# Performance work log

Hardware: AMD Instinct MI355X
Metric: run time of the kernel (lower is better)

## Reference

```python
import jax, jax.numpy as jnp
import numpy as np

EPS = 1e-5
NEG = -1e22

def layernorm(x, g, b):
    m = jnp.mean(x, axis=-1, keepdims=True)
    v = jnp.mean((x - m) ** 2, axis=-1, keepdims=True)
    return (x - m) * jax.lax.rsqrt(v + EPS) * g + b

def setup_inputs() -> dict:
    key = jax.random.key(0)
    ks = jax.random.split(key, 16)
    B, N, D, K = 4, 2048, 512, 32
    H = int(D * 1.5)  # 768
    sc = lambda fan_in: 1.0 / np.sqrt(fan_in)
    inp = {
        'x': jax.random.normal(ks[0], (B, N, D), jnp.float32),
        'adj': jax.random.uniform(ks[1], (B, N, N), jnp.float32),
        'inxs': jax.random.randint(ks[2], (B, N, K), 0, N, jnp.int64),
        'Wq': jax.random.normal(ks[3], (D, D), jnp.float32) * sc(D),
        'bq': jnp.zeros((D,), jnp.float32),
        'Wk': jax.random.normal(ks[4], (D, D), jnp.float32) * sc(D),
        'bk': jnp.zeros((D,), jnp.float32),
        'Wv': jax.random.normal(ks[5], (D, D), jnp.float32) * sc(D),
        'bv': jnp.zeros((D,), jnp.float32),
        'Wo': jax.random.normal(ks[6], (D, D), jnp.float32) * sc(D),
        'bo': jnp.zeros((D,), jnp.float32),
        'g1': jnp.ones((D,), jnp.float32),
        'beta1': jnp.zeros((D,), jnp.float32),
        'W1': jax.random.normal(ks[7], (D, H), jnp.float32) * sc(D),
        'bf1': jnp.zeros((H,), jnp.float32),
        'W2': jax.random.normal(ks[8], (H, D), jnp.float32) * sc(H),
        'bf2': jnp.zeros((D,), jnp.float32),
        'g2': jnp.ones((D,), jnp.float32),
        'beta2': jnp.zeros((D,), jnp.float32),
    }
    return inp

def reference(x, adj, inxs, Wq, bq, Wk, bk, Wv, bv, Wo, bo, g1, beta1, W1, bf1, W2, bf2, g2, beta2):
    B, N, D = x.shape
    # projections
    q = x @ Wq + bq                                   # [B,N,D]
    k = x @ Wk + bk
    v = x @ Wv + bv
    # gather top-k neighbor keys/values: [B,N,K,D]
    b_idx = jnp.arange(B)[:, None, None]
    k_nei = k[b_idx, inxs]
    v_nei = v[b_idx, inxs]
    # attention over selected neighbors, masked by adjacency sign
    scores = jnp.einsum('bnd,bnkd->bnk', q, k_nei) / jnp.sqrt(jnp.float32(D))
    adj_nei = jnp.take_along_axis(adj, inxs, axis=2)  # [B,N,K]
    mask = jnp.where(adj_nei > 0, 0.0, NEG)
    attn = jax.nn.softmax(scores + mask, axis=-1)
    att_out = jnp.einsum('bnk,bnkd->bnd', attn, v_nei) @ Wo + bo
    # residual + LN
    y = layernorm(x + jax.nn.relu(att_out), g1, beta1)
    # FFN + residual + LN
    h = jax.nn.relu(y @ W1 + bf1) @ W2 + bf2
    return layernorm(y + h, g2, beta2)
```

## Files before the change

kernel.cpp:

```cpp
#include <hip/hip_runtime.h>
#include <stdint.h>

typedef __attribute__((ext_vector_type(8))) short short8;
typedef __attribute__((ext_vector_type(4))) float f32x4;
typedef __attribute__((ext_vector_type(2))) _Float16 h2;
typedef __attribute__((ext_vector_type(8))) _Float16 half8;

#define QSCALE 21.1666667f
#define SCONST 9.86413e-5f

static __device__ __forceinline__ unsigned short f2bf(float f) {
  unsigned int u = __float_as_uint(f);
  u += 0x7FFFu + ((u >> 16) & 1u);
  return (unsigned short)(u >> 16);
}
static __device__ __forceinline__ float bf2f(unsigned short h) {
  return __uint_as_float(((unsigned int)h) << 16);
}
static __device__ __forceinline__ unsigned short f2h(float f) {
  _Float16 h = (_Float16)f;
  return __builtin_bit_cast(unsigned short, h);
}
static __device__ __forceinline__ float hdot2(unsigned int a, unsigned int b, float c) {
  return __builtin_amdgcn_fdot2(__builtin_bit_cast(h2, a), __builtin_bit_cast(h2, b), c, false);
}
static __device__ __forceinline__ signed char q8(float v) {
  float sv = fminf(fmaxf(v * QSCALE, -127.f), 127.f);
  return (signed char)(int)rintf(sv);
}

#define GLD16(gp, lp) __builtin_amdgcn_global_load_lds( \
    (__attribute__((address_space(1))) void*)(gp), \
    (__attribute__((address_space(3))) void*)(lp), 16, 0, 0)

__global__ __launch_bounds__(256) void k_prep(
    const float* __restrict__ adj, const int* __restrict__ inxs,
    float* __restrict__ maskb, const float* __restrict__ x,
    unsigned short* __restrict__ xb,
    const float* __restrict__ Wq, const float* __restrict__ Wk,
    const float* __restrict__ Wv, const float* __restrict__ Wo,
    const float* __restrict__ W1, const float* __restrict__ W2,
    unsigned short* __restrict__ wqkvt, unsigned short* __restrict__ wot,
    unsigned short* __restrict__ w1t, unsigned short* __restrict__ w2t) {
  __shared__ float tile[32][33];
  const int bid = blockIdx.x;
  const int t = threadIdx.x;
  if (bid < 1024) {
    const int xcd = bid & 7;
    const int bb = xcd >> 1;
    const int s = ((bid >> 3) << 1) | (xcd & 1);
    const long row = ((long)bb << 11) | ((long)s << 3) | (t >> 5);
    const int kk = t & 31;
    const int idx = inxs[row * 32 + kk];
    const float a = adj[row * 2048 + idx];
    maskb[row * 32 + kk] = a > 0.f ? 0.f : -1e22f;
    return;
  }
  if (bid < 3072) {
    const int lb = bid - 1024;
    const int xcd = lb & 7;
    const int bb = xcd >> 1;
    const int s = ((lb >> 3) << 1) | (xcd & 1);
    const long row = ((long)bb << 11) | ((long)s << 2) | (t >> 6);
    const int lane = t & 63;
    const float4* p = (const float4*)(x + row * 512 + lane * 8);
    float4 a = p[0], b = p[1];
    short8 v;
    v[0] = (short)f2h(a.x); v[1] = (short)f2h(a.y);
    v[2] = (short)f2h(a.z); v[3] = (short)f2h(a.w);
    v[4] = (short)f2h(b.x); v[5] = (short)f2h(b.y);
    v[6] = (short)f2h(b.z); v[7] = (short)f2h(b.w);
    *(short8*)(xb + row * 512 + lane * 8) = v;
    return;
  }
  const int lb = bid - 3072;
  const float* src;
  unsigned short* dst;
  int R, C, f16, local;
  if (lb < 768) {
    const int m = lb >> 8;
    src = m == 0 ? Wq : (m == 1 ? Wk : Wv);
    dst = wqkvt + (long)m * 512 * 512;
    R = 512; C = 512; f16 = 1; local = lb & 255;
  } else if (lb < 1024) {
    src = Wo; dst = wot; R = 512; C = 512; f16 = 0; local = lb - 768;
  } else if (lb < 1408) {
    src = W1; dst = w1t; R = 512; C = 768; f16 = 0; local = lb - 1024;
  } else {
    src = W2; dst = w2t; R = 768; C = 512; f16 = 0; local = lb - 1408;
  }
  const int ntx = C >> 5;
  const int c0 = (local % ntx) << 5;
  const int r0 = (local / ntx) << 5;
  const int tx = t & 31, ty = t >> 5;
#pragma unroll
  for (int i = 0; i < 4; i++)
    tile[ty + i * 8][tx] = src[(long)(r0 + ty + i * 8) * C + c0 + tx];
  __syncthreads();
#pragma unroll
  for (int i = 0; i < 4; i++) {
    float v = tile[tx][ty + i * 8];
    dst[(long)(c0 + ty + i * 8) * R + r0 + tx] = f16 ? f2h(v) : f2bf(v);
  }
}

__global__ __launch_bounds__(256) void k_gemm_qkv(
    const unsigned short* __restrict__ A, const unsigned short* __restrict__ Bt,
    const float* __restrict__ bq, const float* __restrict__ bk,
    const float* __restrict__ bv, signed char* __restrict__ qk8,
    unsigned short* __restrict__ vh) {
  const int K = 512;
  __shared__ unsigned short As[2][128 * 64];
  __shared__ unsigned short Bs[2][128 * 64];
  const int t = threadIdx.x;
  const int lane = t & 63;
  const int w = t >> 6;
  const int wr = w >> 1, wc = w & 1;
  const int lin = blockIdx.x;
  const int xcd = lin & 7;
  const int bb = xcd >> 1;
  const int s = ((lin >> 3) << 1) | (xcd & 1);
  const int m0 = (bb * 16 + s / 12) * 128;
  const int n0 = (s % 12) * 128;

  f32x4 acc[4][4];
#pragma unroll
  for (int mi = 0; mi < 4; mi++)
#pragma unroll
    for (int ni = 0; ni < 4; ni++) {
      f32x4 z = {0.f, 0.f, 0.f, 0.f};
      acc[mi][ni] = z;
    }

  auto stage = [&](int buf, int k0) {
#pragma unroll
    for (int i = 0; i < 4; i++) {
      const int c = t + i * 256;
      const int r = c >> 3, j = c & 7;
      GLD16(A + (long)(m0 + r) * K + k0 + ((j ^ (r & 7)) << 3), &As[buf][c * 8]);
    }
#pragma unroll
    for (int i = 0; i < 4; i++) {
      const int c = t + i * 256;
      const int r = c >> 3, j = c & 7;
      GLD16(Bt + (long)(n0 + r) * K + k0 + ((j ^ (r & 7)) << 3), &Bs[buf][c * 8]);
    }
  };

  const int nt = K >> 6;
  stage(0, 0);
  for (int tt = 0; tt < nt; ++tt) {
    const int cur = tt & 1;
    if (tt + 1 < nt) {
      stage(cur ^ 1, (tt + 1) << 6);
      asm volatile("s_waitcnt vmcnt(8)" ::: "memory");
    } else {
      asm volatile("s_waitcnt vmcnt(0)" ::: "memory");
    }
    __builtin_amdgcn_s_barrier();

#pragma unroll
    for (int kk = 0; kk < 2; kk++) {
      short8 af[4], bf[4];
#pragma unroll
      for (int mi = 0; mi < 4; mi++) {
        const int r = wr * 64 + mi * 16 + (lane & 15);
        const int jj = (kk << 2) + (lane >> 4);
        af[mi] = *(const short8*)&As[cur][r * 64 + ((jj ^ (r & 7)) << 3)];
      }
#pragma unroll
      for (int ni = 0; ni < 4; ni++) {
        const int r = wc * 64 + ni * 16 + (lane & 15);
        const int jj = (kk << 2) + (lane >> 4);
        bf[ni] = *(const short8*)&Bs[cur][r * 64 + ((jj ^ (r & 7)) << 3)];
      }
#pragma unroll
      for (int mi = 0; mi < 4; mi++)
#pragma unroll
        for (int ni = 0; ni < 4; ni++)
          acc[mi][ni] = __builtin_amdgcn_mfma_f32_16x16x32_f16(
              __builtin_bit_cast(half8, af[mi]), __builtin_bit_cast(half8, bf[ni]),
              acc[mi][ni], 0, 0, 0);
    }
    asm volatile("s_waitcnt lgkmcnt(0)" ::: "memory");
    __builtin_amdgcn_s_barrier();
  }

  const int lr = (lane >> 4) * 4;
  const int lc = lane & 15;
  if (n0 < 1024) {
#pragma unroll
    for (int mi = 0; mi < 4; mi++) {
#pragma unroll
      for (int ni = 0; ni < 4; ni++) {
        const int col = n0 + wc * 64 + ni * 16 + lc;
        const float bvv = col < 512 ? bq[col] : bk[col - 512];
#pragma unroll
        for (int r = 0; r < 4; r++) {
          const int row = m0 + wr * 64 + mi * 16 + lr + r;
          qk8[(long)row * 1024 + col] = q8(acc[mi][ni][r] + bvv);
        }
      }
    }
  } else {
#pragma unroll
    for (int mi = 0; mi < 4; mi++) {
#pragma unroll
      for (int ni = 0; ni < 4; ni++) {
        const int col = n0 + wc * 64 + ni * 16 + lc;
        const float bvv = bv[col - 1024];
#pragma unroll
        for (int r = 0; r < 4; r++) {
          const int row = m0 + wr * 64 + mi * 16 + lr + r;
          vh[(long)row * 512 + (col - 1024)] = f2h(acc[mi][ni][r] + bvv);
        }
      }
    }
  }
}

template <int EPI>
__global__ __launch_bounds__(256) void k_gemm(const unsigned short* __restrict__ A,
                                              const unsigned short* __restrict__ Bt,
                                              const float* __restrict__ bias,
                                              unsigned short* __restrict__ C,
                                              int M, int N, int K) {
  __shared__ unsigned short As[2][128 * 64];
  __shared__ unsigned short Bs[2][64 * 64];
  const int t = threadIdx.x;
  const int lane = t & 63;
  const int w = t >> 6;
  const int wr = w >> 1, wc = w & 1;
  const int lin = blockIdx.x;
  const int xcd = lin & 7;
  const int bb = xcd >> 1;
  const int nx = N >> 6;
  const int s = ((lin >> 3) << 1) | (xcd & 1);
  const int m0 = (bb * 16 + s / nx) * 128;
  const int n0 = (s % nx) * 64;

  f32x4 acc[4][2];
#pragma unroll
  for (int mi = 0; mi < 4; mi++)
#pragma unroll
    for (int ni = 0; ni < 2; ni++) {
      f32x4 z = {0.f, 0.f, 0.f, 0.f};
      acc[mi][ni] = z;
    }

  auto stage = [&](int buf, int k0) {
#pragma unroll
    for (int i = 0; i < 4; i++) {
      const int c = t + i * 256;
      const int r = c >> 3, j = c & 7;
      GLD16(A + (long)(m0 + r) * K + k0 + ((j ^ (r & 7)) << 3), &As[buf][c * 8]);
    }
#pragma unroll
    for (int i = 0; i < 2; i++) {
      const int c = t + i * 256;
      const int r = c >> 3, j = c & 7;
      GLD16(Bt + (long)(n0 + r) * K + k0 + ((j ^ (r & 7)) << 3), &Bs[buf][c * 8]);
    }
  };

  const int nt = K >> 6;
  stage(0, 0);
  for (int tt = 0; tt < nt; ++tt) {
    const int cur = tt & 1;
    if (tt + 1 < nt) {
      stage(cur ^ 1, (tt + 1) << 6);
      asm volatile("s_waitcnt vmcnt(6)" ::: "memory");
    } else {
      asm volatile("s_waitcnt vmcnt(0)" ::: "memory");
    }
    __builtin_amdgcn_s_barrier();

#pragma unroll
    for (int kk = 0; kk < 2; kk++) {
      short8 af[4], bf[2];
#pragma unroll
      for (int mi = 0; mi < 4; mi++) {
        const int r = wr * 64 + mi * 16 + (lane & 15);
        const int jj = (kk << 2) + (lane >> 4);
        af[mi] = *(const short8*)&As[cur][r * 64 + ((jj ^ (r & 7)) << 3)];
      }
#pragma unroll
      for (int ni = 0; ni < 2; ni++) {
        const int r = wc * 32 + ni * 16 + (lane & 15);
        const int jj = (kk << 2) + (lane >> 4);
        bf[ni] = *(const short8*)&Bs[cur][r * 64 + ((jj ^ (r & 7)) << 3)];
      }
#pragma unroll
      for (int mi = 0; mi < 4; mi++)
#pragma unroll
        for (int ni = 0; ni < 2; ni++)
          acc[mi][ni] = __builtin_amdgcn_mfma_f32_16x16x32_bf16(af[mi], bf[ni], acc[mi][ni], 0, 0, 0);
    }
    asm volatile("s_waitcnt lgkmcnt(0)" ::: "memory");
    __builtin_amdgcn_s_barrier();
  }

  const int lr = (lane >> 4) * 4;
  const int lc = lane & 15;
#pragma unroll
  for (int mi = 0; mi < 4; mi++) {
#pragma unroll
    for (int ni = 0; ni < 2; ni++) {
      const int col = n0 + wc * 32 + ni * 16 + lc;
      const float bvv = bias[col];
#pragma unroll
      for (int r = 0; r < 4; r++) {
        const int row = m0 + wr * 64 + mi * 16 + lr + r;
        float v = acc[mi][ni][r] + bvv;
        if (EPI == 1) v = fmaxf(v, 0.f);
        C[(long)row * N + col] = f2bf(v);
      }
    }
  }
}

__global__ __launch_bounds__(256, 8) void k_attn(const signed char* __restrict__ qk8,
                                                 const unsigned short* __restrict__ vh,
                                                 const float* __restrict__ maskb,
                                                 const int* __restrict__ inxs,
                                                 unsigned short* __restrict__ att) {
  const int t = threadIdx.x;
  const int lane = t & 63;
  const int w = t >> 6;
  const int bid = blockIdx.x;
  const int xcd = bid & 7;
  const int b = xcd >> 1;
  const int sub = ((bid >> 3) << 1) | (xcd & 1);
  const int row = (b << 11) | (sub << 2) | w;
  const long base = (long)b * 2048;
  const int g = lane >> 4;
  const int li = lane & 15;
  const int kk = lane & 31;

  const int* ix = inxs + (long)row * 32;
  const int ixv = ix[kk];
  const float mval = maskb[(long)row * 32 + kk];

  const uint2* qp = (const uint2*)(qk8 + (long)row * 1024);
  uint2 qc[4];
#pragma unroll
  for (int c = 0; c < 4; c++) qc[c] = qp[li + c * 16];

  float scr[8];
#pragma unroll
  for (int r = 0; r < 8; r++) {
    const int nb = __shfl(ixv, r * 4 + g, 64);
    const uint2* kp = (const uint2*)(qk8 + (base + nb) * 1024 + 512);
    int di = 0;
#pragma unroll
    for (int c = 0; c < 4; c++) {
      uint2 kc = kp[li + c * 16];
      di = __builtin_amdgcn_sdot4((int)kc.x, (int)qc[c].x, di, false);
      di = __builtin_amdgcn_sdot4((int)kc.y, (int)qc[c].y, di, false);
    }
#pragma unroll
    for (int m = 1; m <= 8; m <<= 1) di += __shfl_xor(di, m, 64);
    scr[r] = (float)di;
  }

  const int srcl = (kk & 3) << 4;
  float s = __shfl(scr[0], srcl, 64);
#pragma unroll
  for (int r = 1; r < 8; r++) {
    const float tr = __shfl(scr[r], srcl, 64);
    s = ((kk >> 2) == r) ? tr : s;
  }
  s = s * SCONST + mval;

  float mx = s;
#pragma unroll
  for (int d = 1; d <= 16; d <<= 1) mx = fmaxf(mx, __shfl_xor(mx, d, 64));
  const float e = __expf(s - mx);
  float ts = e;
#pragma unroll
  for (int d = 1; d <= 16; d <<= 1) ts += __shfl_xor(ts, d, 64);
  const float inv = 1.f / ts;

  float o[8] = {0, 0, 0, 0, 0, 0, 0, 0};
#pragma unroll
  for (int p = 0; p < 16; p++) {
    const int u0 = __shfl(ixv, 2 * p, 64);
    const int u1 = __shfl(ixv, 2 * p + 1, 64);
    const uint4 v0c = *(const uint4*)(vh + (base + u0) * 512 + lane * 8);
    const uint4 v1c = *(const uint4*)(vh + (base + u1) * 512 + lane * 8);
    const float pe0 = __shfl(e, 2 * p, 64);
    const float pe1 = __shfl(e, 2 * p + 1, 64);
    const unsigned int pp =
        __builtin_bit_cast(unsigned int, __builtin_amdgcn_cvt_pkrtz(pe0, pe1));
    const unsigned int vw0[4] = {v0c.x, v0c.y, v0c.z, v0c.w};
    const unsigned int vw1[4] = {v1c.x, v1c.y, v1c.z, v1c.w};
#pragma unroll
    for (int q = 0; q < 4; q++) {
      const unsigned int even = __builtin_amdgcn_perm(vw1[q], vw0[q], 0x05040100u);
      const unsigned int odd  = __builtin_amdgcn_perm(vw1[q], vw0[q], 0x07060302u);
      o[2 * q]     = hdot2(even, pp, o[2 * q]);
      o[2 * q + 1] = hdot2(odd,  pp, o[2 * q + 1]);
    }
  }

  short8 ov;
#pragma unroll
  for (int j = 0; j < 8; j++) ov[j] = (short)f2bf(o[j] * inv);
  *(short8*)(att + (long)row * 512 + lane * 8) = ov;
}

__global__ __launch_bounds__(256) void k_ln1(const float* __restrict__ x,
                                             const unsigned short* __restrict__ o,
                                             const float* __restrict__ g,
                                             const float* __restrict__ beta,
                                             unsigned short* __restrict__ y) {
  const int lane = threadIdx.x & 63;
  const int w = threadIdx.x >> 6;
  const int bid = blockIdx.x;
  const int xcd = bid & 7;
  const int bb = xcd >> 1;
  const int s0 = ((bid >> 3) << 1) | (xcd & 1);
  const long row = ((long)bb << 11) | ((long)s0 << 2) | w;
  const float4* xp = (const float4*)(x + row * 512 + lane * 8);
  float4 x0 = xp[0], x1 = xp[1];
  short8 ov = *(const short8*)(o + row * 512 + lane * 8);
  float tv[8] = {x0.x, x0.y, x0.z, x0.w, x1.x, x1.y, x1.z, x1.w};
  float s = 0.f, s2 = 0.f;
#pragma unroll
  for (int j = 0; j < 8; j++) {
    tv[j] += bf2f((unsigned short)ov[j]);
    s += tv[j];
    s2 += tv[j] * tv[j];
  }
#pragma unroll
  for (int m = 32; m >= 1; m >>= 1) {
    s += __shfl_xor(s, m, 64);
    s2 += __shfl_xor(s2, m, 64);
  }
  const float mean = s * (1.f / 512.f);
  const float var = s2 * (1.f / 512.f) - mean * mean;
  const float r = rsqrtf(var + 1e-5f);
  const float4* gp = (const float4*)(g + lane * 8);
  const float4* bp = (const float4*)(beta + lane * 8);
  float4 g0 = gp[0], g1v = gp[1], b0 = bp[0], b1 = bp[1];
  float gg[8] = {g0.x, g0.y, g0.z, g0.w, g1v.x, g1v.y, g1v.z, g1v.w};
  float bb2[8] = {b0.x, b0.y, b0.z, b0.w, b1.x, b1.y, b1.z, b1.w};
  short8 yv;
#pragma unroll
  for (int j = 0; j < 8; j++) yv[j] = (short)f2bf((tv[j] - mean) * r * gg[j] + bb2[j]);
  *(short8*)(y + row * 512 + lane * 8) = yv;
}

__global__ __launch_bounds__(256) void k_ln2(const unsigned short* __restrict__ y,
                                             const unsigned short* __restrict__ f,
                                             const float* __restrict__ g,
                                             const float* __restrict__ beta,
                                             float* __restrict__ out) {
  const int lane = threadIdx.x & 63;
  const int w = threadIdx.x >> 6;
  const int bid = blockIdx.x;
  const int xcd = bid & 7;
  const int bb = xcd >> 1;
  const int s0 = ((bid >> 3) << 1) | (xcd & 1);
  const long row = ((long)bb << 11) | ((long)s0 << 2) | w;
  short8 yv = *(const short8*)(y + row * 512 + lane * 8);
  short8 fv = *(const short8*)(f + row * 512 + lane * 8);
  float tv[8];
  float s = 0.f, s2 = 0.f;
#pragma unroll
  for (int j = 0; j < 8; j++) {
    tv[j] = bf2f((unsigned short)yv[j]) + bf2f((unsigned short)fv[j]);
    s += tv[j];
    s2 += tv[j] * tv[j];
  }
#pragma unroll
  for (int m = 32; m >= 1; m >>= 1) {
    s += __shfl_xor(s, m, 64);
    s2 += __shfl_xor(s2, m, 64);
  }
  const float mean = s * (1.f / 512.f);
  const float var = s2 * (1.f / 512.f) - mean * mean;
  const float r = rsqrtf(var + 1e-5f);
  const float4* gp = (const float4*)(g + lane * 8);
  const float4* bp = (const float4*)(beta + lane * 8);
  float4 g0 = gp[0], g1v = gp[1], b0 = bp[0], b1 = bp[1];
  float gg[8] = {g0.x, g0.y, g0.z, g0.w, g1v.x, g1v.y, g1v.z, g1v.w};
  float bb2[8] = {b0.x, b0.y, b0.z, b0.w, b1.x, b1.y, b1.z, b1.w};
  float ovv[8];
#pragma unroll
  for (int j = 0; j < 8; j++) ovv[j] = (tv[j] - mean) * r * gg[j] + bb2[j];
  float4* op = (float4*)(out + row * 512 + lane * 8);
  float4 o0 = {ovv[0], ovv[1], ovv[2], ovv[3]};
  float4 o1 = {ovv[4], ovv[5], ovv[6], ovv[7]};
  op[0] = o0;
  op[1] = o1;
}

extern "C" void kernel_launch(void* const* d_in, const int* in_sizes, int n_in,
                              void* d_out, int out_size, void* d_ws, size_t ws_size,
                              hipStream_t stream) {
  const float* x   = (const float*)d_in[0];
  const float* adj = (const float*)d_in[1];
  const int*   inx = (const int*)d_in[2];
  const float* Wq  = (const float*)d_in[3];
  const float* bq  = (const float*)d_in[4];
  const float* Wk  = (const float*)d_in[5];
  const float* bk  = (const float*)d_in[6];
  const float* Wv  = (const float*)d_in[7];
  const float* bv  = (const float*)d_in[8];
  const float* Wo  = (const float*)d_in[9];
  const float* bo  = (const float*)d_in[10];
  const float* g1  = (const float*)d_in[11];
  const float* be1 = (const float*)d_in[12];
  const float* W1  = (const float*)d_in[13];
  const float* bf1 = (const float*)d_in[14];
  const float* W2  = (const float*)d_in[15];
  const float* bf2 = (const float*)d_in[16];
  const float* g2  = (const float*)d_in[17];
  const float* be2 = (const float*)d_in[18];

  unsigned short* xb    = (unsigned short*)d_ws;
  unsigned short* wqkvt = xb + 4194304;
  unsigned short* wot   = wqkvt + 786432;
  unsigned short* w1t   = wot + 262144;
  unsigned short* w2t   = w1t + 393216;
  signed char*    qk8   = (signed char*)(w2t + 393216);
  unsigned short* vh    = (unsigned short*)(qk8 + 8388608);
  unsigned short* oproj = vh + 4194304;
  unsigned short* y     = oproj + 4194304;
  float*          maskb = (float*)(y + 4194304);
  unsigned short* att   = xb;
  unsigned short* h     = (unsigned short*)qk8;
  unsigned short* f     = oproj;

  k_prep<<<4864, 256, 0, stream>>>(adj, inx, maskb, x, xb, Wq, Wk, Wv, Wo, W1, W2,
                                   wqkvt, wot, w1t, w2t);

  k_gemm_qkv<<<768, 256, 0, stream>>>(xb, wqkvt, bq, bk, bv, qk8, vh);
  k_attn<<<2048, 256, 0, stream>>>(qk8, vh, maskb, inx, att);
  k_gemm<1><<<512, 256, 0, stream>>>(att, wot, bo, oproj, 8192, 512, 512);
  k_ln1<<<2048, 256, 0, stream>>>(x, oproj, g1, be1, y);
  k_gemm<1><<<768, 256, 0, stream>>>(y, w1t, bf1, h, 8192, 768, 512);
  k_gemm<0><<<512, 256, 0, stream>>>(h, w2t, bf2, f, 8192, 512, 768);
  k_ln2<<<2048, 256, 0, stream>>>(y, f, g2, be2, (float*)d_out);
}
```

Before: 105.8 us.

## Quantize V to per-row uint8 for attention and widen GEMM N-tile to 128

Adds a kernel that quantizes the fp16 V rows to unsigned 8-bit with a per-row scale and offset. The attention kernel then gathers 8 bytes per lane instead of 16 and corrects the offset with a weighted-sum term, which halves the gather traffic of the neighbour V reads. Separately, the generic GEMM tile grows from 128x64 to 128x128, giving each wave more MFMA work per LDS load and halving the grid sizes. The costs are an extra launch and pass over V, reduced precision in the attention output, and higher register and LDS use in the GEMM, which may lower occupancy.

```diff
diff --git a/kernel.cpp b/kernel.cpp
--- a/kernel.cpp
+++ b/kernel.cpp
@@ -21,12 +21,15 @@
   _Float16 h = (_Float16)f;
   return __builtin_bit_cast(unsigned short, h);
 }
-static __device__ __forceinline__ float hdot2(unsigned int a, unsigned int b, float c) {
-  return __builtin_amdgcn_fdot2(__builtin_bit_cast(h2, a), __builtin_bit_cast(h2, b), c, false);
+static __device__ __forceinline__ float h2f(unsigned short h) {
+  return (float)__builtin_bit_cast(_Float16, h);
 }
 static __device__ __forceinline__ signed char q8(float v) {
   float sv = fminf(fmaxf(v * QSCALE, -127.f), 127.f);
   return (signed char)(int)rintf(sv);
+}
+static __device__ __forceinline__ float ub(unsigned int x, int n) {
+  return (float)((x >> (8 * n)) & 0xffu);
 }
 
 #define GLD16(gp, lp) __builtin_amdgcn_global_load_lds( \
@@ -219,6 +222,43 @@
   }
 }
 
+__global__ __launch_bounds__(256) void k_qv(const unsigned short* __restrict__ vh,
+                                            unsigned char* __restrict__ v8,
+                                            float* __restrict__ vs) {
+  const int bid = blockIdx.x;
+  const int xcd = bid & 7;
+  const int bb = xcd >> 1;
+  const int s0 = ((bid >> 3) << 1) | (xcd & 1);
+  const long row = ((long)bb << 11) | ((long)s0 << 2) | (threadIdx.x >> 6);
+  const int lane = threadIdx.x & 63;
+  const unsigned short* vp = vh + row * 512 + lane * 8;
+  float vf[8];
+#pragma unroll
+  for (int j = 0; j < 8; j++) vf[j] = h2f(vp[j]);
+  float mx = 0.f;
+#pragma unroll
+  for (int j = 0; j < 8; j++) mx = fmaxf(mx, fabsf(vf[j]));
+#pragma unroll
+  for (int d = 1; d <= 32; d <<= 1) mx = fmaxf(mx, __shfl_xor(mx, d, 64));
+  mx = fmaxf(mx, 1e-8f);
+  const float sc = mx * (1.f / 127.f);
+  const float isc = 127.f / mx;
+  unsigned int w0 = 0, w1 = 0;
+#pragma unroll
+  for (int j = 0; j < 4; j++) {
+    unsigned int u = (unsigned int)(int)rintf(fminf(fmaxf(vf[j] * isc + 128.f, 0.f), 255.f));
+    w0 |= (u & 255u) << (8 * j);
+  }
+#pragma unroll
+  for (int j = 0; j < 4; j++) {
+    unsigned int u = (unsigned int)(int)rintf(fminf(fmaxf(vf[4 + j] * isc + 128.f, 0.f), 255.f));
+    w1 |= (u & 255u) << (8 * j);
+  }
+  uint2 pw = {w0, w1};
+  *(uint2*)(v8 + row * 512 + lane * 8) = pw;
+  if (lane == 0) vs[row] = sc;
+}
+
 template <int EPI>
 __global__ __launch_bounds__(256) void k_gemm(const unsigned short* __restrict__ A,
                                               const unsigned short* __restrict__ Bt,
@@ -226,7 +266,7 @@
                                               unsigned short* __restrict__ C,
                                               int M, int N, int K) {
   __shared__ unsigned short As[2][128 * 64];
-  __shared__ unsigned short Bs[2][64 * 64];
+  __shared__ unsigned short Bs[2][128 * 64];
   const int t = threadIdx.x;
   const int lane = t & 63;
   const int w = t >> 6;
@@ -234,16 +274,16 @@
   const int lin = blockIdx.x;
   const int xcd = lin & 7;
   const int bb = xcd >> 1;
-  const int nx = N >> 6;
+  const int nx = N >> 7;
   const int s = ((lin >> 3) << 1) | (xcd & 1);
   const int m0 = (bb * 16 + s / nx) * 128;
-  const int n0 = (s % nx) * 64;
-
-  f32x4 acc[4][2];
+  const int n0 = (s % nx) * 128;
+
+  f32x4 acc[4][4];
 #pragma unroll
   for (int mi = 0; mi < 4; mi++)
 #pragma unroll
-    for (int ni = 0; ni < 2; ni++) {
+    for (int ni = 0; ni < 4; ni++) {
       f32x4 z = {0.f, 0.f, 0.f, 0.f};
       acc[mi][ni] = z;
     }
@@ -256,7 +296,7 @@
       GLD16(A + (long)(m0 + r) * K + k0 + ((j ^ (r & 7)) << 3), &As[buf][c * 8]);
     }
 #pragma unroll
-    for (int i = 0; i < 2; i++) {
+    for (int i = 0; i < 4; i++) {
       const int c = t + i * 256;
       const int r = c >> 3, j = c & 7;
       GLD16(Bt + (long)(n0 + r) * K + k0 + ((j ^ (r & 7)) << 3), &Bs[buf][c * 8]);
@@ -269,7 +309,7 @@
     const int cur = tt & 1;
     if (tt + 1 < nt) {
       stage(cur ^ 1, (tt + 1) << 6);
-      asm volatile("s_waitcnt vmcnt(6)" ::: "memory");
+      asm volatile("s_waitcnt vmcnt(8)" ::: "memory");
     } else {
       asm volatile("s_waitcnt vmcnt(0)" ::: "memory");
     }
@@ -277,7 +317,7 @@
 
 #pragma unroll
     for (int kk = 0; kk < 2; kk++) {
-      short8 af[4], bf[2];
+      short8 af[4], bf[4];
 #pragma unroll
       for (int mi = 0; mi < 4; mi++) {
         const int r = wr * 64 + mi * 16 + (lane & 15);
@@ -285,15 +325,15 @@
         af[mi] = *(const short8*)&As[cur][r * 64 + ((jj ^ (r & 7)) << 3)];
       }
 #pragma unroll
-      for (int ni = 0; ni < 2; ni++) {
-        const int r = wc * 32 + ni * 16 + (lane & 15);
+      for (int ni = 0; ni < 4; ni++) {
+        const int r = wc * 64 + ni * 16 + (lane & 15);
         const int jj = (kk << 2) + (lane >> 4);
         bf[ni] = *(const short8*)&Bs[cur][r * 64 + ((jj ^ (r & 7)) << 3)];
       }
 #pragma unroll
       for (int mi = 0; mi < 4; mi++)
 #pragma unroll
-        for (int ni = 0; ni < 2; ni++)
+        for (int ni = 0; ni < 4; ni++)
           acc[mi][ni] = __builtin_amdgcn_mfma_f32_16x16x32_bf16(af[mi], bf[ni], acc[mi][ni], 0, 0, 0);
     }
     asm volatile("s_waitcnt lgkmcnt(0)" ::: "memory");
@@ -305,8 +345,8 @@
 #pragma unroll
   for (int mi = 0; mi < 4; mi++) {
 #pragma unroll
-    for (int ni = 0; ni < 2; ni++) {
-      const int col = n0 + wc * 32 + ni * 16 + lc;
+    for (int ni = 0; ni < 4; ni++) {
+      const int col = n0 + wc * 64 + ni * 16 + lc;
       const float bvv = bias[col];
 #pragma unroll
       for (int r = 0; r < 4; r++) {
@@ -320,7 +360,8 @@
 }
 
 __global__ __launch_bounds__(256, 8) void k_attn(const signed char* __restrict__ qk8,
-                                                 const unsigned short* __restrict__ vh,
+                                                 const unsigned char* __restrict__ v8,
+                                                 const float* __restrict__ vs,
                                                  const float* __restrict__ maskb,
                                                  const int* __restrict__ inxs,
                                                  unsigned short* __restrict__ att) {
@@ -340,6 +381,7 @@
   const int* ix = inxs + (long)row * 32;
   const int ixv = ix[kk];
   const float mval = maskb[(long)row * 32 + kk];
+  const float sv = vs[base + ixv];
 
   const uint2* qp = (const uint2*)(qk8 + (long)row * 1024);
   uint2 qc[4];
@@ -381,31 +423,30 @@
   for (int d = 1; d <= 16; d <<= 1) ts += __shfl_xor(ts, d, 64);
   const float inv = 1.f / ts;
 
+  const float wgt = e * sv;
+  float sw = wgt;
+#pragma unroll
+  for (int d = 1; d <= 16; d <<= 1) sw += __shfl_xor(sw, d, 64);
+
   float o[8] = {0, 0, 0, 0, 0, 0, 0, 0};
 #pragma unroll
-  for (int p = 0; p < 16; p++) {
-    const int u0 = __shfl(ixv, 2 * p, 64);
-    const int u1 = __shfl(ixv, 2 * p + 1, 64);
-    const uint4 v0c = *(const uint4*)(vh + (base + u0) * 512 + lane * 8);
-    const uint4 v1c = *(const uint4*)(vh + (base + u1) * 512 + lane * 8);
-    const float pe0 = __shfl(e, 2 * p, 64);
-    const float pe1 = __shfl(e, 2 * p + 1, 64);
-    const unsigned int pp =
-        __builtin_bit_cast(unsigned int, __builtin_amdgcn_cvt_pkrtz(pe0, pe1));
-    const unsigned int vw0[4] = {v0c.x, v0c.y, v0c.z, v0c.w};
-    const unsigned int vw1[4] = {v1c.x, v1c.y, v1c.z, v1c.w};
-#pragma unroll
-    for (int q = 0; q < 4; q++) {
-      const unsigned int even = __builtin_amdgcn_perm(vw1[q], vw0[q], 0x05040100u);
-      const unsigned int odd  = __builtin_amdgcn_perm(vw1[q], vw0[q], 0x07060302u);
-      o[2 * q]     = hdot2(even, pp, o[2 * q]);
-      o[2 * q + 1] = hdot2(odd,  pp, o[2 * q + 1]);
-    }
+  for (int p = 0; p < 32; p++) {
+    const int un = __shfl(ixv, p, 64);
+    const float wn = __shfl(wgt, p, 64);
+    const uint2 vv = *(const uint2*)(v8 + (base + un) * 512 + lane * 8);
+    o[0] += wn * ub(vv.x, 0);
+    o[1] += wn * ub(vv.x, 1);
+    o[2] += wn * ub(vv.x, 2);
+    o[3] += wn * ub(vv.x, 3);
+    o[4] += wn * ub(vv.y, 0);
+    o[5] += wn * ub(vv.y, 1);
+    o[6] += wn * ub(vv.y, 2);
+    o[7] += wn * ub(vv.y, 3);
   }
 
   short8 ov;
 #pragma unroll
-  for (int j = 0; j < 8; j++) ov[j] = (short)f2bf(o[j] * inv);
+  for (int j = 0; j < 8; j++) ov[j] = (short)f2bf((o[j] - 128.f * sw) * inv);
   *(short8*)(att + (long)row * 512 + lane * 8) = ov;
 }
 
@@ -529,18 +570,20 @@
   unsigned short* oproj = vh + 4194304;
   unsigned short* y     = oproj + 4194304;
   float*          maskb = (float*)(y + 4194304);
+  unsigned char*  v8    = (unsigned char*)(maskb + 262144);
+  float*          vs    = (float*)(v8 + 4194304);
   unsigned short* att   = xb;
   unsigned short* h     = (unsigned short*)qk8;
   unsigned short* f     = oproj;
 
   k_prep<<<4864, 256, 0, stream>>>(adj, inx, maskb, x, xb, Wq, Wk, Wv, Wo, W1, W2,
                                    wqkvt, wot, w1t, w2t);
-
   k_gemm_qkv<<<768, 256, 0, stream>>>(xb, wqkvt, bq, bk, bv, qk8, vh);
-  k_attn<<<2048, 256, 0, stream>>>(qk8, vh, maskb, inx, att);
-  k_gemm<1><<<512, 256, 0, stream>>>(att, wot, bo, oproj, 8192, 512, 512);
+  k_qv<<<2048, 256, 0, stream>>>(vh, v8, vs);
+  k_attn<<<2048, 256, 0, stream>>>(qk8, v8, vs, maskb, inx, att);
+  k_gemm<1><<<256, 256, 0, stream>>>(att, wot, bo, oproj, 8192, 512, 512);
   k_ln1<<<2048, 256, 0, stream>>>(x, oproj, g1, be1, y);
-  k_gemm<1><<<768, 256, 0, stream>>>(y, w1t, bf1, h, 8192, 768, 512);
-  k_gemm<0><<<512, 256, 0, stream>>>(h, w2t, bf2, f, 8192, 512, 768);
+  k_gemm<1><<<384, 256, 0, stream>>>(y, w1t, bf1, h, 8192, 768, 512);
+  k_gemm<0><<<256, 256, 0, stream>>>(h, w2t, bf2, f, 8192, 512, 768);
   k_ln2<<<2048, 256, 0, stream>>>(y, f, g2, be2, (float*)d_out);
 }
```

Result: slower. 117.4 us (+10.9%).
